# Kernel optimization log

Measured on AMD Instinct MI355X. Metric: run time of the kernel, lower is better.

## Reference

```python
import jax, jax.numpy as jnp
import numpy as np

B, N = 32, 512
N_DIM, N_P, N_K = 128, 3, 2
F0_DIM = N_DIM * N_P            # 384
CAT_DIM = N_DIM * (N_K + 1) * N_P  # 1152


def setup_inputs() -> dict:
    key = jax.random.key(0)
    ks = jax.random.split(key, 12)
    s = 0.05
    return {
        "loc": jax.random.uniform(ks[0], (B, N, 2), dtype=jnp.float32),
        "deadline": jax.random.uniform(ks[1], (B, N), dtype=jnp.float32),
        "workload": jax.random.uniform(ks[2], (B, N), dtype=jnp.float32),
        "depot": jax.random.uniform(ks[3], (B, 1, 2), dtype=jnp.float32),
        "W_init": jax.random.normal(ks[4], (3, F0_DIM), dtype=jnp.float32) * s,
        "b_init": jnp.zeros((F0_DIM,), jnp.float32),
        "W_dep": jax.random.normal(ks[5], (2, N_DIM), dtype=jnp.float32) * s,
        "b_dep": jnp.zeros((N_DIM,), jnp.float32),
        "W_g1": jax.random.normal(ks[6], (CAT_DIM, N_DIM), dtype=jnp.float32) * s,
        "b_g1": jnp.zeros((N_DIM,), jnp.float32),
        "W_g2": jax.random.normal(ks[7], (CAT_DIM, N_DIM), dtype=jnp.float32) * s,
        "b_g2": jnp.zeros((N_DIM,), jnp.float32),
        "W_g3": jax.random.normal(ks[8], (CAT_DIM, N_DIM), dtype=jnp.float32) * s,
        "b_g3": jnp.zeros((N_DIM,), jnp.float32),
        "gamma": jnp.ones((F0_DIM,), jnp.float32),
        "beta": jnp.zeros((F0_DIM,), jnp.float32),
        "W_F": jax.random.normal(ks[9], (F0_DIM, N_DIM), dtype=jnp.float32) * s,
        "b_F": jnp.zeros((N_DIM,), jnp.float32),
    }


def _forward(loc, deadline, workload, depot, W_init, b_init, W_dep, b_dep,
             W_g1, b_g1, W_g2, b_g2, W_g3, b_g3, gamma, beta, W_F, b_F):
    # X = [loc, deadline/deadline.max()] -> [B,N,3] (workload is concatenated then dropped in original)
    X = jnp.concatenate([loc, (deadline / deadline.max())[..., None]], axis=-1)
    n = X.shape[1]
    # pairwise squared distances [B,N,N]
    d2 = ((X[:, :, None, :] - X[:, None, :, :]) ** 2).sum(-1)
    off = ~jnp.eye(n, dtype=bool)                      # off-diagonal mask
    d2_safe = jnp.where(off, d2, 1.0)
    A = jnp.where(off, 1.0 / jnp.sqrt(d2_safe), 0.0)   # A = 1/dist off-diag, 0 on diag
    A = jnp.where(jnp.isnan(A), 0.0, A)                # A[A!=A]=0
    A = A / A.max()                                    # global max-normalize
    deg = A.sum(-1) - 1.0                              # (A.sum(-1) - 1)
    L = jnp.eye(n, dtype=A.dtype) * deg[:, None, :] - A  # D - A (diag = deg)
    L2 = L @ L

    F0 = X @ W_init + b_init                           # [B,N,384]
    F0_sq = F0 * F0
    F0_cu = F0 * F0_sq

    def prop(F):
        return jnp.concatenate([F, L @ F, L2 @ F], axis=-1)  # [B,N,1152]

    g1 = prop(F0) @ W_g1 + b_g1
    g2 = prop(F0_sq) @ W_g2 + b_g2
    g3 = prop(F0_cu) @ W_g3 + b_g3
    F1 = jnp.concatenate([g1, g2, g3], axis=-1)        # [B,N,384]
    F1 = jax.nn.leaky_relu(F1) + F0

    # BatchNorm1d (training mode): stats over flattened (B*N) samples, biased var
    flat = F1.reshape(-1, F1.shape[-1])
    mu = flat.mean(0)
    var = ((flat - mu) ** 2).mean(0)
    F1 = (F1 - mu) / jnp.sqrt(var + 1e-5) * gamma + beta

    F_final = jax.nn.leaky_relu(F1 @ W_F + b_F)        # [B,N,128]
    dep = depot @ W_dep + b_dep                        # [B,1,128]
    h = jnp.concatenate([dep, F_final], axis=1)        # [B,N+1,128]
    return h, h.mean(axis=1)


def reference(loc, deadline, workload, depot, W_init, b_init, W_dep, b_dep,
              W_g1, b_g1, W_g2, b_g2, W_g3, b_g3, gamma, beta, W_F, b_F):
    return _forward(loc, deadline, workload, depot, W_init, b_init, W_dep, b_dep,
                    W_g1, b_g1, W_g2, b_g2, W_g3, b_g3, gamma, beta, W_F, b_F)
```

## Files before the change

kernel.cpp:

```cpp
#include <hip/hip_runtime.h>

#define LEAKY(x) ((x) > 0.0f ? (x) : 0.01f * (x))

typedef __attribute__((ext_vector_type(8))) short bf16x8;
typedef __attribute__((ext_vector_type(4))) float f32x4;
typedef __attribute__((ext_vector_type(4))) unsigned short u16x4;

__device__ __forceinline__ unsigned short f2bf(float f) {
    unsigned int u = __float_as_uint(f);
    unsigned int r = (u + 0x7fffu + ((u >> 16) & 1u)) >> 16;
    return (unsigned short)r;
}
__device__ __forceinline__ float bf2f(unsigned short u) {
    return __uint_as_float(((unsigned int)u) << 16);
}

__device__ __forceinline__ void dma16(const unsigned short* g, unsigned short* l) {
    __builtin_amdgcn_global_load_lds(
        (const __attribute__((address_space(1))) void*)g,
        (__attribute__((address_space(3))) void*)l, 16, 0, 0);
}


__global__ void k_dmax(const float* __restrict__ deadline, float* __restrict__ dmax) {
    __shared__ float red[256];
    int t = threadIdx.x;
    float m = -1e30f;
    for (int i = t; i < 16384; i += 256) m = fmaxf(m, deadline[i]);
    red[t] = m; __syncthreads();
    for (int s = 128; s > 0; s >>= 1) {
        if (t < s) red[t] = fmaxf(red[t], red[t + s]);
        __syncthreads();
    }
    if (t == 0) *dmax = red[0];
}

__global__ __launch_bounds__(256) void k_buildR(const float* __restrict__ loc,
                                                const float* __restrict__ deadline,
                                                const float* __restrict__ dmaxv,
                                                float* __restrict__ R,
                                                float* __restrict__ rowsum, float* __restrict__ pmax) {
    int blk = blockIdx.x;
    int wave = threadIdx.x >> 6, lane = threadIdx.x & 63;
    int bi = blk * 4 + wave;
    int b = bi >> 9, i = bi & 511;
    float invd = 1.0f / (*dmaxv);
    const float* lb = loc + b * 1024;
    const float* db = deadline + b * 512;
    float xi = lb[i * 2], yi = lb[i * 2 + 1], zi = db[i] * invd;
    float lsum = 0.f, lmax = 0.f;
    float* Rrow = R + (size_t)bi * 512;
    for (int j = lane; j < 512; j += 64) {
        float d0 = xi - lb[j * 2], d1 = yi - lb[j * 2 + 1], d2 = zi - db[j] * invd;
        float dd = d0 * d0 + d1 * d1 + d2 * d2;
        float r = (j == i) ? 0.f : rsqrtf(dd);
        Rrow[j] = r;
        lsum += r; lmax = fmaxf(lmax, r);
    }
    for (int off = 32; off > 0; off >>= 1) {
        lsum += __shfl_down(lsum, off);
        lmax = fmaxf(lmax, __shfl_down(lmax, off));
    }
    __shared__ float smax[4];
    if (lane == 0) { rowsum[bi] = lsum; smax[wave] = lmax; }
    __syncthreads();
    if (threadIdx.x == 0) pmax[blk] = fmaxf(fmaxf(smax[0], smax[1]), fmaxf(smax[2], smax[3]));
}

__global__ void k_amax(const float* __restrict__ pmax, float* __restrict__ amaxf) {
    __shared__ float red[256];
    int t = threadIdx.x;
    float m = 0.f;
    for (int i = t; i < 4096; i += 256) m = fmaxf(m, pmax[i]);
    red[t] = m; __syncthreads();
    for (int s = 128; s > 0; s >>= 1) {
        if (t < s) red[t] = fmaxf(red[t], red[t + s]);
        __syncthreads();
    }
    if (t == 0) *amaxf = red[0];
}

__global__ void k_buildL(const float* __restrict__ R, const float* __restrict__ rowsum,
                         const float* __restrict__ amaxf, unsigned short* __restrict__ Lb) {
    int id = blockIdx.x * 256 + threadIdx.x;
    float inv = 1.0f / (*amaxf);
    size_t e = (size_t)id * 4;
    size_t bi = e >> 9;
    int i = (int)(bi & 511);
    int j0 = (int)(e & 511);
    float4 rv = *(const float4*)(R + e);
    float diag = rowsum[bi] * inv - 1.0f;
    u16x4 o;
    o[0] = f2bf(i == j0     ? diag : -rv.x * inv);
    o[1] = f2bf(i == j0 + 1 ? diag : -rv.y * inv);
    o[2] = f2bf(i == j0 + 2 ? diag : -rv.z * inv);
    o[3] = f2bf(i == j0 + 3 ? diag : -rv.w * inv);
    *(u16x4*)(Lb + e) = o;
}

__global__ void k_F0pow(const float* __restrict__ loc, const float* __restrict__ deadline,
                        const float* __restrict__ dmaxv,
                        const float* __restrict__ Wi, const float* __restrict__ bi_,
                        unsigned short* __restrict__ P1, unsigned short* __restrict__ P2,
                        unsigned short* __restrict__ P3) {
    int id = blockIdx.x * 256 + threadIdx.x;
    int row = id / 384, c = id % 384;
    float x0 = loc[row * 2], x1 = loc[row * 2 + 1], x2 = deadline[row] / (*dmaxv);
    float f = x0 * Wi[c] + x1 * Wi[384 + c] + x2 * Wi[768 + c] + bi_[c];
    P1[id] = f2bf(f);
    P2[id] = f2bf(f * f);
    P3[id] = f2bf(f * f * f);
}

__global__ void k_prepW(const float* __restrict__ Wg1, const float* __restrict__ Wg2,
                        const float* __restrict__ Wg3, unsigned short* __restrict__ WgT) {
    int id = blockIdx.x * 256 + threadIdx.x;
    int combo = id / 49152, rem = id % 49152;
    int n = rem / 384, k = rem % 384;
    int kp = combo / 3, part = combo % 3;
    const float* W = (kp == 0) ? Wg1 : (kp == 1 ? Wg2 : Wg3);
    WgT[id] = f2bf(W[(part * 384 + k) * 128 + n]);
}


__device__ __forceinline__ void gemm_phase(
    const unsigned short* __restrict__ Ab, int Astr,
    const unsigned short* __restrict__ Bb, int Bstr,
    int ksteps,
    unsigned short* AsL, unsigned short* BsL,
    f32x4 (&acc)[4][4], int t)
{
    const int wave = t >> 6, lane = t & 63;
    const int wm = wave >> 1, wn = wave & 1;
    const int quad = lane >> 4, l16 = lane & 15;
    const int lrow = lane >> 2, lkq = (lane & 3) * 8;
    const int c0 = wave, c1 = wave + 4;
    for (int s = 0; s < ksteps; s++) {
        __syncthreads();
        int k0 = s * 32;
        dma16(Ab + (size_t)(c0 * 16 + lrow) * Astr + k0 + lkq, AsL + c0 * 512);
        dma16(Ab + (size_t)(c1 * 16 + lrow) * Astr + k0 + lkq, AsL + c1 * 512);
        dma16(Bb + (size_t)(c0 * 16 + lrow) * Bstr + k0 + lkq, BsL + c0 * 512);
        dma16(Bb + (size_t)(c1 * 16 + lrow) * Bstr + k0 + lkq, BsL + c1 * 512);
        __syncthreads();
        bf16x8 af[4], bf[4];
#pragma unroll
        for (int i = 0; i < 4; i++)
            af[i] = *(const bf16x8*)(AsL + (wm * 64 + i * 16 + l16) * 32 + quad * 8);
#pragma unroll
        for (int n = 0; n < 4; n++)
            bf[n] = *(const bf16x8*)(BsL + (wn * 64 + n * 16 + l16) * 32 + quad * 8);
#pragma unroll
        for (int i = 0; i < 4; i++)
#pragma unroll
            for (int n = 0; n < 4; n++)
                acc[i][n] = __builtin_amdgcn_mfma_f32_16x16x32_bf16(af[i], bf[n], acc[i][n], 0, 0, 0);
    }
}

__global__ __launch_bounds__(256) void k_ygemmT(
    const unsigned short* __restrict__ WgT,
    const unsigned short* __restrict__ P1, const unsigned short* __restrict__ P2,
    const unsigned short* __restrict__ P3, unsigned short* __restrict__ Y2T)
{
    __shared__ unsigned short AsL[4096], BsL[4096];
    const int t = threadIdx.x;
    const int kp = blockIdx.x;
    const int nb = blockIdx.y;
    const int b = blockIdx.z;
    const unsigned short* P = (kp == 0) ? P1 : (kp == 1 ? P2 : P3);
    const unsigned short* Ab = WgT + (size_t)(kp * 3 + 2) * 49152;
    const unsigned short* Bb = P + ((size_t)b * 512 + nb * 128) * 384;
    f32x4 acc[4][4];
#pragma unroll
    for (int i = 0; i < 4; i++)
#pragma unroll
        for (int n = 0; n < 4; n++) acc[i][n] = (f32x4){0.f, 0.f, 0.f, 0.f};
    gemm_phase(Ab, 384, Bb, 384, 12, AsL, BsL, acc, t);

    const int wave = t >> 6, lane = t & 63;
    const int wm = wave >> 1, wn = wave & 1;
    const int quad = lane >> 4, l16 = lane & 15;
#pragma unroll
    for (int i = 0; i < 4; i++)
#pragma unroll
        for (int n = 0; n < 4; n++) {
            int g = kp * 128 + wm * 64 + i * 16 + quad * 4;
            int node = nb * 128 + wn * 64 + n * 16 + l16;
#pragma unroll
            for (int r = 0; r < 4; r++)
                Y2T[((size_t)b * 384 + g + r) * 512 + node] = f2bf(acc[i][n][r]);
        }
}

__global__ __launch_bounds__(256) void k_lg1T(
    const unsigned short* __restrict__ Lb, const unsigned short* __restrict__ Y2T,
    const unsigned short* __restrict__ WgT,
    const unsigned short* __restrict__ P1, const unsigned short* __restrict__ P2,
    const unsigned short* __restrict__ P3, unsigned short* __restrict__ ZT)
{
    __shared__ unsigned short AsL[4096], BsL[4096];
    const int t = threadIdx.x;
    const int kp = blockIdx.x;
    const int nb = blockIdx.y;
    const int b = blockIdx.z;
    const unsigned short* P = (kp == 0) ? P1 : (kp == 1 ? P2 : P3);
    f32x4 acc[4][4];
#pragma unroll
    for (int i = 0; i < 4; i++)
#pragma unroll
        for (int n = 0; n < 4; n++) acc[i][n] = (f32x4){0.f, 0.f, 0.f, 0.f};
    gemm_phase(Y2T + (size_t)b * 196608 + (size_t)kp * 128 * 512, 512,
               Lb + (size_t)b * 262144 + (size_t)nb * 128 * 512, 512,
               16, AsL, BsL, acc, t);
    gemm_phase(WgT + (size_t)(kp * 3 + 1) * 49152, 384,
               P + ((size_t)b * 512 + nb * 128) * 384, 384,
               12, AsL, BsL, acc, t);

    const int wave = t >> 6, lane = t & 63;
    const int wm = wave >> 1, wn = wave & 1;
    const int quad = lane >> 4, l16 = lane & 15;
#pragma unroll
    for (int i = 0; i < 4; i++)
#pragma unroll
        for (int n = 0; n < 4; n++) {
            int g = kp * 128 + wm * 64 + i * 16 + quad * 4;
            int node = nb * 128 + wn * 64 + n * 16 + l16;
#pragma unroll
            for (int r = 0; r < 4; r++)
                ZT[((size_t)b * 384 + g + r) * 512 + node] = f2bf(acc[i][n][r]);
        }
}

__global__ __launch_bounds__(256) void k_lg2(
    const unsigned short* __restrict__ Lb, const unsigned short* __restrict__ ZT,
    const unsigned short* __restrict__ WgT,
    const unsigned short* __restrict__ P1, const unsigned short* __restrict__ P2,
    const unsigned short* __restrict__ P3,
    const float* __restrict__ bg1, const float* __restrict__ bg2, const float* __restrict__ bg3,
    unsigned short* __restrict__ F1b, float* __restrict__ bn1, float* __restrict__ bn2)
{
    __shared__ unsigned short AsL[4096], BsL[4096];
    __shared__ float bnS[128], bnQ[128];
    const int t = threadIdx.x;
    const int mb = blockIdx.x;
    const int kp = blockIdx.y;
    const int b = blockIdx.z;
    if (t < 128) { bnS[t] = 0.f; bnQ[t] = 0.f; }
    const unsigned short* P = (kp == 0) ? P1 : (kp == 1 ? P2 : P3);
    f32x4 acc[4][4];
#pragma unroll
    for (int i = 0; i < 4; i++)
#pragma unroll
        for (int n = 0; n < 4; n++) acc[i][n] = (f32x4){0.f, 0.f, 0.f, 0.f};
    gemm_phase(Lb + (size_t)b * 262144 + (size_t)mb * 128 * 512, 512,
               ZT + (size_t)b * 196608 + (size_t)kp * 128 * 512, 512,
               16, AsL, BsL, acc, t);
    gemm_phase(P + ((size_t)b * 512 + mb * 128) * 384, 384,
               WgT + (size_t)(kp * 3 + 0) * 49152, 384,
               12, AsL, BsL, acc, t);

    const int wave = t >> 6, lane = t & 63;
    const int wm = wave >> 1, wn = wave & 1;
    const int quad = lane >> 4, l16 = lane & 15;
    const float* bg = (kp == 0) ? bg1 : (kp == 1 ? bg2 : bg3);
    float ls1[4], ls2[4];
#pragma unroll
    for (int n = 0; n < 4; n++) { ls1[n] = 0.f; ls2[n] = 0.f; }
#pragma unroll
    for (int i = 0; i < 4; i++) {
        int rowl = mb * 128 + wm * 64 + i * 16 + quad * 4;
        size_t rowg = (size_t)b * 512 + rowl;
#pragma unroll
        for (int n = 0; n < 4; n++) {
            int colloc = wn * 64 + n * 16 + l16;
            int g = kp * 128 + colloc;
            float bias = bg[colloc];
#pragma unroll
            for (int r = 0; r < 4; r++) {
                size_t idx = (rowg + r) * 384 + g;
                float c = acc[i][n][r] + bias;
                float v = LEAKY(c) + bf2f(P1[idx]);
                F1b[idx] = f2bf(v);
                ls1[n] += v; ls2[n] += v * v;
            }
        }
    }
#pragma unroll
    for (int n = 0; n < 4; n++) {
        int colloc = wn * 64 + n * 16 + l16;
        atomicAdd(&bnS[colloc], ls1[n]);
        atomicAdd(&bnQ[colloc], ls2[n]);
    }
    __syncthreads();
    if (t < 128) {
        atomicAdd(&bn1[kp * 128 + t], bnS[t]);
        atomicAdd(&bn2[kp * 128 + t], bnQ[t]);
    }
}

__global__ __launch_bounds__(384) void k_bnfin_beff(
    const float* __restrict__ bn1, const float* __restrict__ bn2,
    const float* __restrict__ gamma, const float* __restrict__ beta,
    const float* __restrict__ WF, const float* __restrict__ bF,
    float* __restrict__ sS, float* __restrict__ beffv)
{
    __shared__ float ttL[384];
    int c = threadIdx.x;
    float mu = bn1[c] * (1.f / 16384.f);
    float var = bn2[c] * (1.f / 16384.f) - mu * mu;
    float sc = gamma[c] / sqrtf(var + 1e-5f);
    sS[c] = sc;
    ttL[c] = beta[c] - mu * sc;
    __syncthreads();
    if (c < 128) {
        float a = bF[c];
        for (int k = 0; k < 384; k++) a += ttL[k] * WF[k * 128 + c];
        beffv[c] = a;
    }
}

__global__ void k_fold(const float* __restrict__ WF, const float* __restrict__ sS,
                       unsigned short* __restrict__ WFsT) {
    int id = blockIdx.x * 256 + threadIdx.x;
    int n = id / 384, k = id % 384;
    WFsT[id] = f2bf(WF[k * 128 + n] * sS[k]);
}

__global__ __launch_bounds__(256) void k_fgemm(
    const unsigned short* __restrict__ F1b, const unsigned short* __restrict__ WFsT,
    const float* __restrict__ beffv, float* __restrict__ out, float* __restrict__ msum)
{
    __shared__ unsigned short AsL[4096], BsL[4096];
    __shared__ float msS[128];
    const int t = threadIdx.x;
    const int mb = blockIdx.x;
    if (t < 128) msS[t] = 0.f;
    f32x4 acc[4][4];
#pragma unroll
    for (int i = 0; i < 4; i++)
#pragma unroll
        for (int n = 0; n < 4; n++) acc[i][n] = (f32x4){0.f, 0.f, 0.f, 0.f};
    gemm_phase(F1b + (size_t)mb * 128 * 384, 384, WFsT, 384, 12, AsL, BsL, acc, t);

    const int wave = t >> 6, lane = t & 63;
    const int wm = wave >> 1, wn = wave & 1;
    const int quad = lane >> 4, l16 = lane & 15;
    const int bloc = mb >> 2;
    float ls[4];
#pragma unroll
    for (int n = 0; n < 4; n++) ls[n] = 0.f;
#pragma unroll
    for (int i = 0; i < 4; i++) {
        int rowg = mb * 128 + wm * 64 + i * 16 + quad * 4;
        int nd = rowg & 511;
#pragma unroll
        for (int n = 0; n < 4; n++) {
            int col = wn * 64 + n * 16 + l16;
            float bb = beffv[col];
#pragma unroll
            for (int r = 0; r < 4; r++) {
                float x = acc[i][n][r] + bb;
                float v = LEAKY(x);
                out[(size_t)bloc * 65664 + (size_t)(nd + r + 1) * 128 + col] = v;
                ls[n] += v;
            }
        }
    }
#pragma unroll
    for (int n = 0; n < 4; n++) atomicAdd(&msS[wn * 64 + n * 16 + l16], ls[n]);
    __syncthreads();
    if (t < 128) atomicAdd(&msum[bloc * 128 + t], msS[t]);
}

__global__ void k_meandep(const float* __restrict__ depot, const float* __restrict__ Wd,
                          const float* __restrict__ bd, const float* __restrict__ msum,
                          float* __restrict__ out) {
    int id = blockIdx.x * 256 + threadIdx.x;
    int b = id >> 7, o = id & 127;
    float dep = depot[b * 2] * Wd[o] + depot[b * 2 + 1] * Wd[128 + o] + bd[o];
    out[(size_t)b * 65664 + o] = dep;
    out[2101248 + id] = (msum[id] + dep) * (1.0f / 513.0f);
}


extern "C" void kernel_launch(void* const* d_in, const int* in_sizes, int n_in,
                              void* d_out, int out_size, void* d_ws, size_t ws_size,
                              hipStream_t stream) {
    const float* loc      = (const float*)d_in[0];
    const float* deadline = (const float*)d_in[1];
    const float* depot    = (const float*)d_in[3];
    const float* W_init   = (const float*)d_in[4];
    const float* b_init   = (const float*)d_in[5];
    const float* W_dep    = (const float*)d_in[6];
    const float* b_dep    = (const float*)d_in[7];
    const float* W_g1     = (const float*)d_in[8];
    const float* b_g1     = (const float*)d_in[9];
    const float* W_g2     = (const float*)d_in[10];
    const float* b_g2     = (const float*)d_in[11];
    const float* W_g3     = (const float*)d_in[12];
    const float* b_g3     = (const float*)d_in[13];
    const float* gamma    = (const float*)d_in[14];
    const float* beta     = (const float*)d_in[15];
    const float* W_F      = (const float*)d_in[16];
    const float* b_F      = (const float*)d_in[17];
    float* out = (float*)d_out;
    float* ws  = (float*)d_ws;

    float* dmaxv  = ws + 0;
    float* amaxf  = ws + 4;
    float* bn1    = ws + 8;
    float* bn2    = ws + 392;
    float* msum   = ws + 776;
    float* rowsum = ws + 4872;
    float* pmax   = ws + 21256;
    float* sS     = ws + 25352;
    float* beffv  = ws + 25736;
    float* R      = ws + 25864;
    unsigned short* Lb   = (unsigned short*)(ws + 8414472);
    unsigned short* P1   = (unsigned short*)(ws + 12608776);
    unsigned short* P2   = (unsigned short*)(ws + 15754504);
    unsigned short* P3   = (unsigned short*)(ws + 18900232);
    unsigned short* WgT  = (unsigned short*)(ws + 22045960);
    unsigned short* WFsT = (unsigned short*)(ws + 22267144);
    unsigned short* Y2T  = (unsigned short*)(ws + 22291720);
    unsigned short* ZT   = (unsigned short*)(ws + 25437448);
    unsigned short* F1b  = (unsigned short*)(ws + 28583176);

    hipMemsetAsync(bn1, 0, (384 + 384 + 4096) * sizeof(float), stream);

    k_dmax<<<1, 256, 0, stream>>>(deadline, dmaxv);
    k_buildR<<<4096, 256, 0, stream>>>(loc, deadline, dmaxv, R, rowsum, pmax);
    k_amax<<<1, 256, 0, stream>>>(pmax, amaxf);
    k_buildL<<<8192, 256, 0, stream>>>(R, rowsum, amaxf, Lb);
    k_F0pow<<<24576, 256, 0, stream>>>(loc, deadline, dmaxv, W_init, b_init, P1, P2, P3);
    k_prepW<<<1728, 256, 0, stream>>>(W_g1, W_g2, W_g3, WgT);

    k_ygemmT<<<dim3(3, 4, 32), 256, 0, stream>>>(WgT, P1, P2, P3, Y2T);
    k_lg1T<<<dim3(3, 4, 32), 256, 0, stream>>>(Lb, Y2T, WgT, P1, P2, P3, ZT);
    k_lg2<<<dim3(4, 3, 32), 256, 0, stream>>>(Lb, ZT, WgT, P1, P2, P3,
                                              b_g1, b_g2, b_g3, F1b, bn1, bn2);

    k_bnfin_beff<<<1, 384, 0, stream>>>(bn1, bn2, gamma, beta, W_F, b_F, sS, beffv);
    k_fold<<<192, 256, 0, stream>>>(W_F, sS, WFsT);
    k_fgemm<<<128, 256, 0, stream>>>(F1b, WFsT, beffv, out, msum);
    k_meandep<<<16, 256, 0, stream>>>(depot, W_dep, b_dep, msum, out);
}
```

Before: 266.4 us.

## Shrink GEMM tiles to raise block count, deepen K step, vectorize F0pow

```diff
diff --git a/kernel.cpp b/kernel.cpp
--- a/kernel.cpp
+++ b/kernel.cpp
@@ -104,12 +104,23 @@
                         unsigned short* __restrict__ P1, unsigned short* __restrict__ P2,
                         unsigned short* __restrict__ P3) {
     int id = blockIdx.x * 256 + threadIdx.x;
-    int row = id / 384, c = id % 384;
+    int row = id / 96, c4 = (id % 96) * 4;
     float x0 = loc[row * 2], x1 = loc[row * 2 + 1], x2 = deadline[row] / (*dmaxv);
-    float f = x0 * Wi[c] + x1 * Wi[384 + c] + x2 * Wi[768 + c] + bi_[c];
-    P1[id] = f2bf(f);
-    P2[id] = f2bf(f * f);
-    P3[id] = f2bf(f * f * f);
+    float4 w0 = *(const float4*)(Wi + c4);
+    float4 w1 = *(const float4*)(Wi + 384 + c4);
+    float4 w2 = *(const float4*)(Wi + 768 + c4);
+    float4 bb = *(const float4*)(bi_ + c4);
+    float f[4] = {x0 * w0.x + x1 * w1.x + x2 * w2.x + bb.x,
+                  x0 * w0.y + x1 * w1.y + x2 * w2.y + bb.y,
+                  x0 * w0.z + x1 * w1.z + x2 * w2.z + bb.z,
+                  x0 * w0.w + x1 * w1.w + x2 * w2.w + bb.w};
+    u16x4 o1, o2, o3;
+#pragma unroll
+    for (int j = 0; j < 4; j++) {
+        o1[j] = f2bf(f[j]); o2[j] = f2bf(f[j] * f[j]); o3[j] = f2bf(f[j] * f[j] * f[j]);
+    }
+    size_t e = (size_t)row * 384 + c4;
+    *(u16x4*)(P1 + e) = o1; *(u16x4*)(P2 + e) = o2; *(u16x4*)(P3 + e) = o3;
 }
 
 __global__ void k_prepW(const float* __restrict__ Wg1, const float* __restrict__ Wg2,
@@ -123,38 +134,83 @@
 }
 
 
-__device__ __forceinline__ void gemm_phase(
+__device__ __forceinline__ void phase128x64(
     const unsigned short* __restrict__ Ab, int Astr,
     const unsigned short* __restrict__ Bb, int Bstr,
-    int ksteps,
-    unsigned short* AsL, unsigned short* BsL,
-    f32x4 (&acc)[4][4], int t)
+    int kiters, unsigned short* AsL, unsigned short* BsL,
+    f32x4 (&acc)[4][2], int t)
 {
     const int wave = t >> 6, lane = t & 63;
     const int wm = wave >> 1, wn = wave & 1;
     const int quad = lane >> 4, l16 = lane & 15;
     const int lrow = lane >> 2, lkq = (lane & 3) * 8;
-    const int c0 = wave, c1 = wave + 4;
-    for (int s = 0; s < ksteps; s++) {
+    for (int s = 0; s < kiters; s++) {
         __syncthreads();
-        int k0 = s * 32;
-        dma16(Ab + (size_t)(c0 * 16 + lrow) * Astr + k0 + lkq, AsL + c0 * 512);
-        dma16(Ab + (size_t)(c1 * 16 + lrow) * Astr + k0 + lkq, AsL + c1 * 512);
-        dma16(Bb + (size_t)(c0 * 16 + lrow) * Bstr + k0 + lkq, BsL + c0 * 512);
-        dma16(Bb + (size_t)(c1 * 16 + lrow) * Bstr + k0 + lkq, BsL + c1 * 512);
+        int k0 = s * 64;
+#pragma unroll
+        for (int h = 0; h < 2; h++) {
+            const unsigned short* Ah = Ab + k0 + h * 32 + lkq;
+            unsigned short* Ap = AsL + h * 4096;
+            dma16(Ah + (size_t)(wave * 16 + lrow) * Astr, Ap + wave * 512);
+            dma16(Ah + (size_t)((wave + 4) * 16 + lrow) * Astr, Ap + (wave + 4) * 512);
+            dma16(Bb + k0 + h * 32 + lkq + (size_t)(wave * 16 + lrow) * Bstr,
+                  BsL + h * 2048 + wave * 512);
+        }
         __syncthreads();
-        bf16x8 af[4], bf[4];
-#pragma unroll
-        for (int i = 0; i < 4; i++)
-            af[i] = *(const bf16x8*)(AsL + (wm * 64 + i * 16 + l16) * 32 + quad * 8);
-#pragma unroll
-        for (int n = 0; n < 4; n++)
-            bf[n] = *(const bf16x8*)(BsL + (wn * 64 + n * 16 + l16) * 32 + quad * 8);
-#pragma unroll
-        for (int i = 0; i < 4; i++)
-#pragma unroll
-            for (int n = 0; n < 4; n++)
-                acc[i][n] = __builtin_amdgcn_mfma_f32_16x16x32_bf16(af[i], bf[n], acc[i][n], 0, 0, 0);
+#pragma unroll
+        for (int h = 0; h < 2; h++) {
+            bf16x8 af[4], bfr[2];
+#pragma unroll
+            for (int i = 0; i < 4; i++)
+                af[i] = *(const bf16x8*)(AsL + h * 4096 + (wm * 64 + i * 16 + l16) * 32 + quad * 8);
+#pragma unroll
+            for (int n = 0; n < 2; n++)
+                bfr[n] = *(const bf16x8*)(BsL + h * 2048 + (wn * 32 + n * 16 + l16) * 32 + quad * 8);
+#pragma unroll
+            for (int i = 0; i < 4; i++)
+#pragma unroll
+                for (int n = 0; n < 2; n++)
+                    acc[i][n] = __builtin_amdgcn_mfma_f32_16x16x32_bf16(af[i], bfr[n], acc[i][n], 0, 0, 0);
+        }
+    }
+}
+
+__device__ __forceinline__ void phase64x64(
+    const unsigned short* __restrict__ Ab, int Astr,
+    const unsigned short* __restrict__ Bb, int Bstr,
+    int kiters, unsigned short* AsL, unsigned short* BsL,
+    f32x4 (&acc)[2][2], int t)
+{
+    const int wave = t >> 6, lane = t & 63;
+    const int wm = wave >> 1, wn = wave & 1;
+    const int quad = lane >> 4, l16 = lane & 15;
+    const int lrow = lane >> 2, lkq = (lane & 3) * 8;
+    for (int s = 0; s < kiters; s++) {
+        __syncthreads();
+        int k0 = s * 64;
+#pragma unroll
+        for (int h = 0; h < 2; h++) {
+            dma16(Ab + k0 + h * 32 + lkq + (size_t)(wave * 16 + lrow) * Astr,
+                  AsL + h * 2048 + wave * 512);
+            dma16(Bb + k0 + h * 32 + lkq + (size_t)(wave * 16 + lrow) * Bstr,
+                  BsL + h * 2048 + wave * 512);
+        }
+        __syncthreads();
+#pragma unroll
+        for (int h = 0; h < 2; h++) {
+            bf16x8 af[2], bfr[2];
+#pragma unroll
+            for (int i = 0; i < 2; i++)
+                af[i] = *(const bf16x8*)(AsL + h * 2048 + (wm * 32 + i * 16 + l16) * 32 + quad * 8);
+#pragma unroll
+            for (int n = 0; n < 2; n++)
+                bfr[n] = *(const bf16x8*)(BsL + h * 2048 + (wn * 32 + n * 16 + l16) * 32 + quad * 8);
+#pragma unroll
+            for (int i = 0; i < 2; i++)
+#pragma unroll
+                for (int n = 0; n < 2; n++)
+                    acc[i][n] = __builtin_amdgcn_mfma_f32_16x16x32_bf16(af[i], bfr[n], acc[i][n], 0, 0, 0);
+        }
     }
 }
 
@@ -163,20 +219,19 @@
     const unsigned short* __restrict__ P1, const unsigned short* __restrict__ P2,
     const unsigned short* __restrict__ P3, unsigned short* __restrict__ Y2T)
 {
-    __shared__ unsigned short AsL[4096], BsL[4096];
+    __shared__ unsigned short AsL[8192], BsL[4096];
     const int t = threadIdx.x;
     const int kp = blockIdx.x;
     const int nb = blockIdx.y;
     const int b = blockIdx.z;
     const unsigned short* P = (kp == 0) ? P1 : (kp == 1 ? P2 : P3);
-    const unsigned short* Ab = WgT + (size_t)(kp * 3 + 2) * 49152;
-    const unsigned short* Bb = P + ((size_t)b * 512 + nb * 128) * 384;
-    f32x4 acc[4][4];
+    f32x4 acc[4][2];
 #pragma unroll
     for (int i = 0; i < 4; i++)
 #pragma unroll
-        for (int n = 0; n < 4; n++) acc[i][n] = (f32x4){0.f, 0.f, 0.f, 0.f};
-    gemm_phase(Ab, 384, Bb, 384, 12, AsL, BsL, acc, t);
+        for (int n = 0; n < 2; n++) acc[i][n] = (f32x4){0.f, 0.f, 0.f, 0.f};
+    phase128x64(WgT + (size_t)(kp * 3 + 2) * 49152, 384,
+                P + ((size_t)b * 512 + nb * 64) * 384, 384, 6, AsL, BsL, acc, t);
 
     const int wave = t >> 6, lane = t & 63;
     const int wm = wave >> 1, wn = wave & 1;
@@ -184,9 +239,9 @@
 #pragma unroll
     for (int i = 0; i < 4; i++)
 #pragma unroll
-        for (int n = 0; n < 4; n++) {
+        for (int n = 0; n < 2; n++) {
             int g = kp * 128 + wm * 64 + i * 16 + quad * 4;
-            int node = nb * 128 + wn * 64 + n * 16 + l16;
+            int node = nb * 64 + wn * 32 + n * 16 + l16;
 #pragma unroll
             for (int r = 0; r < 4; r++)
                 Y2T[((size_t)b * 384 + g + r) * 512 + node] = f2bf(acc[i][n][r]);
@@ -199,23 +254,21 @@
     const unsigned short* __restrict__ P1, const unsigned short* __restrict__ P2,
     const unsigned short* __restrict__ P3, unsigned short* __restrict__ ZT)
 {
-    __shared__ unsigned short AsL[4096], BsL[4096];
+    __shared__ unsigned short AsL[8192], BsL[4096];
     const int t = threadIdx.x;
     const int kp = blockIdx.x;
     const int nb = blockIdx.y;
     const int b = blockIdx.z;
     const unsigned short* P = (kp == 0) ? P1 : (kp == 1 ? P2 : P3);
-    f32x4 acc[4][4];
+    f32x4 acc[4][2];
 #pragma unroll
     for (int i = 0; i < 4; i++)
 #pragma unroll
-        for (int n = 0; n < 4; n++) acc[i][n] = (f32x4){0.f, 0.f, 0.f, 0.f};
-    gemm_phase(Y2T + (size_t)b * 196608 + (size_t)kp * 128 * 512, 512,
-               Lb + (size_t)b * 262144 + (size_t)nb * 128 * 512, 512,
-               16, AsL, BsL, acc, t);
-    gemm_phase(WgT + (size_t)(kp * 3 + 1) * 49152, 384,
-               P + ((size_t)b * 512 + nb * 128) * 384, 384,
-               12, AsL, BsL, acc, t);
+        for (int n = 0; n < 2; n++) acc[i][n] = (f32x4){0.f, 0.f, 0.f, 0.f};
+    phase128x64(Y2T + (size_t)b * 196608 + (size_t)kp * 128 * 512, 512,
+                Lb + (size_t)b * 262144 + (size_t)nb * 64 * 512, 512, 8, AsL, BsL, acc, t);
+    phase128x64(WgT + (size_t)(kp * 3 + 1) * 49152, 384,
+                P + ((size_t)b * 512 + nb * 64) * 384, 384, 6, AsL, BsL, acc, t);
 
     const int wave = t >> 6, lane = t & 63;
     const int wm = wave >> 1, wn = wave & 1;
@@ -223,9 +276,9 @@
 #pragma unroll
     for (int i = 0; i < 4; i++)
 #pragma unroll
-        for (int n = 0; n < 4; n++) {
+        for (int n = 0; n < 2; n++) {
             int g = kp * 128 + wm * 64 + i * 16 + quad * 4;
-            int node = nb * 128 + wn * 64 + n * 16 + l16;
+            int node = nb * 64 + wn * 32 + n * 16 + l16;
 #pragma unroll
             for (int r = 0; r < 4; r++)
                 ZT[((size_t)b * 384 + g + r) * 512 + node] = f2bf(acc[i][n][r]);
@@ -240,42 +293,41 @@
     const float* __restrict__ bg1, const float* __restrict__ bg2, const float* __restrict__ bg3,
     unsigned short* __restrict__ F1b, float* __restrict__ bn1, float* __restrict__ bn2)
 {
-    __shared__ unsigned short AsL[4096], BsL[4096];
-    __shared__ float bnS[128], bnQ[128];
+    __shared__ unsigned short AsL[8192], BsL[4096];
+    __shared__ float bnS[64], bnQ[64];
     const int t = threadIdx.x;
     const int mb = blockIdx.x;
-    const int kp = blockIdx.y;
+    const int gt = blockIdx.y;
     const int b = blockIdx.z;
-    if (t < 128) { bnS[t] = 0.f; bnQ[t] = 0.f; }
+    const int kp = gt >> 1;
+    if (t < 64) { bnS[t] = 0.f; bnQ[t] = 0.f; }
     const unsigned short* P = (kp == 0) ? P1 : (kp == 1 ? P2 : P3);
-    f32x4 acc[4][4];
+    f32x4 acc[4][2];
 #pragma unroll
     for (int i = 0; i < 4; i++)
 #pragma unroll
-        for (int n = 0; n < 4; n++) acc[i][n] = (f32x4){0.f, 0.f, 0.f, 0.f};
-    gemm_phase(Lb + (size_t)b * 262144 + (size_t)mb * 128 * 512, 512,
-               ZT + (size_t)b * 196608 + (size_t)kp * 128 * 512, 512,
-               16, AsL, BsL, acc, t);
-    gemm_phase(P + ((size_t)b * 512 + mb * 128) * 384, 384,
-               WgT + (size_t)(kp * 3 + 0) * 49152, 384,
-               12, AsL, BsL, acc, t);
+        for (int n = 0; n < 2; n++) acc[i][n] = (f32x4){0.f, 0.f, 0.f, 0.f};
+    phase128x64(Lb + (size_t)b * 262144 + (size_t)mb * 128 * 512, 512,
+                ZT + (size_t)b * 196608 + (size_t)gt * 64 * 512, 512, 8, AsL, BsL, acc, t);
+    phase128x64(P + ((size_t)b * 512 + mb * 128) * 384, 384,
+                WgT + (size_t)(kp * 3) * 49152 + (size_t)(gt & 1) * 64 * 384, 384, 6, AsL, BsL, acc, t);
 
     const int wave = t >> 6, lane = t & 63;
     const int wm = wave >> 1, wn = wave & 1;
     const int quad = lane >> 4, l16 = lane & 15;
     const float* bg = (kp == 0) ? bg1 : (kp == 1 ? bg2 : bg3);
-    float ls1[4], ls2[4];
-#pragma unroll
-    for (int n = 0; n < 4; n++) { ls1[n] = 0.f; ls2[n] = 0.f; }
+    float ls1[2], ls2[2];
+#pragma unroll
+    for (int n = 0; n < 2; n++) { ls1[n] = 0.f; ls2[n] = 0.f; }
 #pragma unroll
     for (int i = 0; i < 4; i++) {
         int rowl = mb * 128 + wm * 64 + i * 16 + quad * 4;
         size_t rowg = (size_t)b * 512 + rowl;
 #pragma unroll
-        for (int n = 0; n < 4; n++) {
-            int colloc = wn * 64 + n * 16 + l16;
-            int g = kp * 128 + colloc;
-            float bias = bg[colloc];
+        for (int n = 0; n < 2; n++) {
+            int nloc = wn * 32 + n * 16 + l16;
+            int g = gt * 64 + nloc;
+            float bias = bg[(gt & 1) * 64 + nloc];
 #pragma unroll
             for (int r = 0; r < 4; r++) {
                 size_t idx = (rowg + r) * 384 + g;
@@ -287,15 +339,15 @@
         }
     }
 #pragma unroll
-    for (int n = 0; n < 4; n++) {
-        int colloc = wn * 64 + n * 16 + l16;
-        atomicAdd(&bnS[colloc], ls1[n]);
-        atomicAdd(&bnQ[colloc], ls2[n]);
+    for (int n = 0; n < 2; n++) {
+        int nloc = wn * 32 + n * 16 + l16;
+        atomicAdd(&bnS[nloc], ls1[n]);
+        atomicAdd(&bnQ[nloc], ls2[n]);
     }
     __syncthreads();
-    if (t < 128) {
-        atomicAdd(&bn1[kp * 128 + t], bnS[t]);
-        atomicAdd(&bn2[kp * 128 + t], bnQ[t]);
+    if (t < 64) {
+        atomicAdd(&bn1[gt * 64 + t], bnS[t]);
+        atomicAdd(&bn2[gt * 64 + t], bnQ[t]);
     }
 }
 
@@ -332,31 +384,34 @@
     const float* __restrict__ beffv, float* __restrict__ out, float* __restrict__ msum)
 {
     __shared__ unsigned short AsL[4096], BsL[4096];
-    __shared__ float msS[128];
+    __shared__ float msS[64];
     const int t = threadIdx.x;
     const int mb = blockIdx.x;
-    if (t < 128) msS[t] = 0.f;
-    f32x4 acc[4][4];
-#pragma unroll
-    for (int i = 0; i < 4; i++)
-#pragma unroll
-        for (int n = 0; n < 4; n++) acc[i][n] = (f32x4){0.f, 0.f, 0.f, 0.f};
-    gemm_phase(F1b + (size_t)mb * 128 * 384, 384, WFsT, 384, 12, AsL, BsL, acc, t);
+    const int nt = blockIdx.y;
+    if (t < 64) msS[t] = 0.f;
+    f32x4 acc[2][2];
+#pragma unroll
+    for (int i = 0; i < 2; i++)
+#pragma unroll
+        for (int n = 0; n < 2; n++) acc[i][n] = (f32x4){0.f, 0.f, 0.f, 0.f};
+    phase64x64(F1b + (size_t)mb * 64 * 384, 384,
+               WFsT + (size_t)nt * 64 * 384, 384, 6, AsL, BsL, acc, t);
 
     const int wave = t >> 6, lane = t & 63;
     const int wm = wave >> 1, wn = wave & 1;
     const int quad = lane >> 4, l16 = lane & 15;
-    const int bloc = mb >> 2;
-    float ls[4];
-#pragma unroll
-    for (int n = 0; n < 4; n++) ls[n] = 0.f;
-#pragma unroll
-    for (int i = 0; i < 4; i++) {
-        int rowg = mb * 128 + wm * 64 + i * 16 + quad * 4;
+    const int bloc = mb >> 3;
+    float ls[2];
+#pragma unroll
+    for (int n = 0; n < 2; n++) ls[n] = 0.f;
+#pragma unroll
+    for (int i = 0; i < 2; i++) {
+        int rowg = mb * 64 + wm * 32 + i * 16 + quad * 4;
         int nd = rowg & 511;
 #pragma unroll
-        for (int n = 0; n < 4; n++) {
-            int col = wn * 64 + n * 16 + l16;
+        for (int n = 0; n < 2; n++) {
+            int nloc = wn * 32 + n * 16 + l16;
+            int col = nt * 64 + nloc;
             float bb = beffv[col];
 #pragma unroll
             for (int r = 0; r < 4; r++) {
@@ -368,9 +423,9 @@
         }
     }
 #pragma unroll
-    for (int n = 0; n < 4; n++) atomicAdd(&msS[wn * 64 + n * 16 + l16], ls[n]);
+    for (int n = 0; n < 2; n++) atomicAdd(&msS[wn * 32 + n * 16 + l16], ls[n]);
     __syncthreads();
-    if (t < 128) atomicAdd(&msum[bloc * 128 + t], msS[t]);
+    if (t < 64) atomicAdd(&msum[bloc * 128 + nt * 64 + t], msS[t]);
 }
 
 __global__ void k_meandep(const float* __restrict__ depot, const float* __restrict__ Wd,
@@ -433,16 +488,16 @@
     k_buildR<<<4096, 256, 0, stream>>>(loc, deadline, dmaxv, R, rowsum, pmax);
     k_amax<<<1, 256, 0, stream>>>(pmax, amaxf);
     k_buildL<<<8192, 256, 0, stream>>>(R, rowsum, amaxf, Lb);
-    k_F0pow<<<24576, 256, 0, stream>>>(loc, deadline, dmaxv, W_init, b_init, P1, P2, P3);
+    k_F0pow<<<6144, 256, 0, stream>>>(loc, deadline, dmaxv, W_init, b_init, P1, P2, P3);
     k_prepW<<<1728, 256, 0, stream>>>(W_g1, W_g2, W_g3, WgT);
 
-    k_ygemmT<<<dim3(3, 4, 32), 256, 0, stream>>>(WgT, P1, P2, P3, Y2T);
-    k_lg1T<<<dim3(3, 4, 32), 256, 0, stream>>>(Lb, Y2T, WgT, P1, P2, P3, ZT);
-    k_lg2<<<dim3(4, 3, 32), 256, 0, stream>>>(Lb, ZT, WgT, P1, P2, P3,
+    k_ygemmT<<<dim3(3, 8, 32), 256, 0, stream>>>(WgT, P1, P2, P3, Y2T);
+    k_lg1T<<<dim3(3, 8, 32), 256, 0, stream>>>(Lb, Y2T, WgT, P1, P2, P3, ZT);
+    k_lg2<<<dim3(4, 6, 32), 256, 0, stream>>>(Lb, ZT, WgT, P1, P2, P3,
                                               b_g1, b_g2, b_g3, F1b, bn1, bn2);
 
     k_bnfin_beff<<<1, 384, 0, stream>>>(bn1, bn2, gamma, beta, W_F, b_F, sS, beffv);
     k_fold<<<192, 256, 0, stream>>>(W_F, sS, WFsT);
-    k_fgemm<<<128, 256, 0, stream>>>(F1b, WFsT, beffv, out, msum);
+    k_fgemm<<<dim3(256, 2), 256, 0, stream>>>(F1b, WFsT, beffv, out, msum);
     k_meandep<<<16, 256, 0, stream>>>(depot, W_dep, b_dep, msum, out);
 }
```

Result: no change. 265.7 us (-0.3%).
